# Performance work log

Hardware: AMD Instinct MI355X
Metric: run time of the kernel (lower is better)

The kernel has to match this reference:

```python
import jax, jax.numpy as jnp
import numpy as np
from jax.scipy.special import logsumexp

DEPTH = 7
LOG_EPS = jnp.float32(-64.0)
EPS = jnp.float32(np.exp(-64.0))


def leaf_interval(depth, start_idx=0):
    if depth == 0:
        return ([start_idx], [start_idx], [], start_idx)
    l_l, l_r, l_adj, last = leaf_interval(depth - 1, start_idx)
    my = last + 1
    r_l, r_r, r_adj, last = leaf_interval(depth - 1, my + 1)
    return ([my] + l_l, [my] + r_r,
            [(l, r) for l in l_r for r in r_l] + l_adj + r_adj, last)


_start, _end, _adj, _ = leaf_interval(DEPTH)
_out_idx = np.array([i for i, _ in _adj], dtype=np.int32)
OUT_UNIQ, OUT_INV = np.unique(_out_idx, return_inverse=True)
IN_IDX = np.array([j for _, j in _adj], dtype=np.int32)
START_IDXS = np.array(_start, dtype=np.int32)
END_IDXS = np.array(_end, dtype=np.int32)
N_STATES = 2 ** (DEPTH + 1) - 1  # 255


def log_safe(x):
    m = x < EPS
    return jnp.where(m, LOG_EPS, jnp.log(jnp.where(m, EPS, x)))


def exp_safe(x):
    m = x < LOG_EPS
    return jnp.where(m, EPS, jnp.exp(jnp.where(m, LOG_EPS, x)))


def setup_inputs() -> dict:
    key = jax.random.key(0)
    k1, k2, k3 = jax.random.split(key, 3)
    V, B, vocab, T = N_STATES, 64, 5000, 50
    log_probs = jax.nn.log_softmax(
        jax.random.normal(k1, (V, B, vocab), dtype=jnp.float32), axis=-1)
    targets = jax.random.randint(k2, (T, B), 0, vocab)
    target_lengths = jax.random.randint(k3, (B,), 1, T + 1)
    return {"log_probs": log_probs, "targets": targets,
            "target_lengths": target_lengths}


def _forward_ctreec(extracted, target_lengths):
    # extracted: [T, B, V] time-major per-state label log-probs
    T, B, V = extracted.shape
    out_uniq = jnp.asarray(OUT_UNIQ)
    out_inv = jnp.asarray(OUT_INV)
    in_idx = jnp.asarray(IN_IDX)
    end_idxs = jnp.asarray(END_IDXS)
    prev0 = jnp.zeros((B, V), jnp.float32).at[:, jnp.asarray(START_IDXS)].set(1.0)
    acc0 = jnp.zeros((B,), jnp.float32)

    def step(carry, xs):
        prev_probs, acc = carry
        elp_t, t = xs
        log_curr = log_safe(prev_probs) + elp_t            # [B, V]
        log_out = log_curr[:, out_uniq]                    # [B, U] unique out nodes
        log_C = logsumexp(log_out, axis=-1, keepdims=True)  # [B, 1]
        outgoing = exp_safe(log_out - log_C)[:, out_inv]   # [B, E] per-edge probs
        end = (t + 1) == target_lengths                    # [B]
        end_vals = logsumexp(log_curr[:, end_idxs], axis=1)
        acc = acc + jnp.where(end, end_vals, 0.0)
        mid = ((t + 1) < target_lengths) & (t < T - 1)
        acc = acc + jnp.where(mid, log_C[:, 0], 0.0)
        # scatter-add outgoing edge mass onto destination nodes
        new_prev = jnp.zeros_like(prev_probs).at[:, in_idx].add(outgoing)
        return (new_prev, acc), None

    (_, acc), _ = jax.lax.scan(step, (prev0, acc0),
                               (extracted, jnp.arange(T)))
    return acc


def reference(log_probs, targets, target_lengths):
    V, B, vocab = log_probs.shape
    # extracted[t, b, v] = log_probs[v, b, targets[t, b]]
    extracted = log_probs[:, jnp.arange(B)[None, :], targets]  # [V, T, B]
    extracted = jnp.transpose(extracted, (1, 2, 0))            # [T, B, V]
    return -_forward_ctreec(extracted, target_lengths)
```

## Files before the change

### kernel.cpp

```cpp
#include <hip/hip_runtime.h>
#include <math.h>


#define TT 50
#define BB 64
#define VOCAB 5000
#define NS 255
#define NSP 256
#define LOG_EPS_F (-64.0f)
#define EPS_F 1.6038109389511818e-28f
#define WS_NEEDED ((size_t)BB * TT * NSP * 4)

__device__ __forceinline__ float wred_sum(float x) {
#pragma unroll
    for (int m = 32; m >= 1; m >>= 1) x += __shfl_xor(x, m);
    return x;
}
__device__ __forceinline__ float wred_max(float x) {
#pragma unroll
    for (int m = 32; m >= 1; m >>= 1) x = fmaxf(x, __shfl_xor(x, m));
    return x;
}

__global__ __launch_bounds__(256) void gather_kernel(
    const float* __restrict__ log_probs,
    const int* __restrict__ targets,
    const int* __restrict__ target_lengths,
    float* __restrict__ ews)
{
    const int bt = blockIdx.x;
    const int b = bt / TT;
    const int t = bt % TT;
    if (t >= target_lengths[b]) return;
    const int v = threadIdx.x;
    const int tgt = targets[t * BB + b];
    float val = 0.0f;
    if (v < NS)
        val = __expf(log_probs[(size_t)v * (BB * VOCAB) + (size_t)b * VOCAB + tgt]);
    ews[(size_t)bt * NSP + v] = val;
}

__global__ __launch_bounds__(64) void scan_kernel(
    const float* __restrict__ ews,
    const int* __restrict__ target_lengths,
    float* __restrict__ out)
{
    const int b = blockIdx.x;
    const int lane = threadIdx.x;
    const int vbase = lane * 4;
    __shared__ float outv[NSP];

    const int len = target_lengths[b];
    const float4* ew = (const float4*)(ews + (size_t)b * TT * NSP);

    bool isend[4], isout[4];
    int kk[4], jj[4];
    float prev[4];
#pragma unroll
    for (int i = 0; i < 4; ++i) {
        int v = vbase + i;
        int p = v + 1;
        bool valid = (v < NS);
        bool pw2 = (p & (p - 1)) == 0;
        bool e_ = valid && ((p + (p & (-p))) == 256);
        isend[i] = e_;
        isout[i] = valid && !e_;
        prev[i] = (valid && pw2) ? 1.0f : 0.0f;
        if (valid && !pw2) {
            int s = __ffs(p) - 1;
            int q = p & (p - 1);
            kk[i] = __ffs(q) - 1;
            jj[i] = v - (1 << s);
        } else { kk[i] = 0; jj[i] = 0; }
    }

    float acc = 0.0f;
    float4 eA = ew[lane];
    float4 eB = (len > 1) ? ew[64 + lane] : eA;
    for (int t = 0; t < len; ++t) {
        float4 cur = eA;
        eA = eB;
        if (t + 2 < len) eB = ew[(t + 2) * 64 + lane];

        float c[4];
        c[0] = prev[0] * cur.x;
        c[1] = prev[1] * cur.y;
        c[2] = prev[2] * cur.z;
        c[3] = prev[3] * cur.w;

        if (t == len - 1) {
            float s = 0.0f;
#pragma unroll
            for (int i = 0; i < 4; ++i)
                if (isend[i]) s += c[i];
            s = wred_sum(s);
            acc += __logf(s);
        } else {
            *(float4*)&outv[vbase] = make_float4(c[0], c[1], c[2], c[3]);
            float s = 0.0f;
#pragma unroll
            for (int i = 0; i < 4; ++i)
                if (isout[i]) s += c[i];
            s = wred_sum(s);
            acc += __logf(s);
            float rinv = 1.0f / s;
            __syncthreads();
#pragma unroll
            for (int i = 0; i < 4; ++i) {
                float np_ = 0.0f;
                int bj = jj[i];
                int n = kk[i];
                for (int a = 0; a < n; ++a) np_ += outv[bj - (1 << a)];
                prev[i] = np_ * rinv;
            }
            __syncthreads();
        }
    }
    if (lane == 0) out[b] = -acc;
}

__global__ __launch_bounds__(64) void ctreec_fused(
    const float* __restrict__ log_probs,
    const int* __restrict__ targets,
    const int* __restrict__ target_lengths,
    float* __restrict__ out)
{
    const int b = blockIdx.x;
    const int lane = threadIdx.x;
    const int vbase = lane * 4;
    __shared__ float e_lds[TT * NSP];
    __shared__ float outv[NSP];
    __shared__ int tgts[TT];
    const int len = target_lengths[b];
    if (lane < TT) tgts[lane] = targets[lane * BB + b];
    __syncthreads();
    {
        const size_t bvoff = (size_t)b * VOCAB;
        float4* e_vec = (float4*)e_lds;
#pragma unroll 4
        for (int t = 0; t < len; ++t) {
            const float* base = log_probs + bvoff + (size_t)tgts[t];
            float4 val;
            val.x = base[(size_t)(vbase + 0) * (BB * VOCAB)];
            val.y = base[(size_t)(vbase + 1) * (BB * VOCAB)];
            val.z = base[(size_t)(vbase + 2) * (BB * VOCAB)];
            val.w = (vbase + 3 < NS) ? base[(size_t)(vbase + 3) * (BB * VOCAB)] : -1e30f;
            e_vec[t * 64 + lane] = val;
        }
    }
    __syncthreads();
    bool isend[4], isout[4];
    int kk[4], jj[4];
    float prev[4];
#pragma unroll
    for (int i = 0; i < 4; ++i) {
        int v = vbase + i;
        int p = v + 1;
        bool valid = (v < NS);
        bool pw2 = (p & (p - 1)) == 0;
        bool e_ = valid && ((p + (p & (-p))) == 256);
        isend[i] = e_;
        isout[i] = valid && !e_;
        prev[i] = (valid && pw2) ? 1.0f : 0.0f;
        if (valid && !pw2) {
            int s = __ffs(p) - 1;
            int q = p & (p - 1);
            kk[i] = __ffs(q) - 1;
            jj[i] = v - (1 << s);
        } else { kk[i] = 0; jj[i] = 0; }
    }
    const float4* e_vec = (const float4*)e_lds;
    float acc = 0.0f;
    for (int t = 0; t < len; ++t) {
        float4 e4 = e_vec[t * 64 + lane];
        float e[4] = {e4.x, e4.y, e4.z, e4.w};
        float lc[4];
#pragma unroll
        for (int i = 0; i < 4; ++i) {
            float pv = prev[i];
            float lp = (pv < EPS_F) ? LOG_EPS_F : __logf(pv);
            lc[i] = lp + e[i];
        }
        if (t == len - 1) {
            float m = -INFINITY;
#pragma unroll
            for (int i = 0; i < 4; ++i)
                if (isend[i]) m = fmaxf(m, lc[i]);
            m = wred_max(m);
            float s = 0.0f;
#pragma unroll
            for (int i = 0; i < 4; ++i)
                if (isend[i]) s += __expf(lc[i] - m);
            s = wred_sum(s);
            acc += m + __logf(s);
        } else {
            float m = -INFINITY;
#pragma unroll
            for (int i = 0; i < 4; ++i)
                if (isout[i]) m = fmaxf(m, lc[i]);
            m = wred_max(m);
            float s = 0.0f;
#pragma unroll
            for (int i = 0; i < 4; ++i)
                if (isout[i]) s += __expf(lc[i] - m);
            s = wred_sum(s);
            float logC = m + __logf(s);
            acc += logC;
#pragma unroll
            for (int i = 0; i < 4; ++i) {
                float d = lc[i] - logC;
                outv[vbase + i] = (d < LOG_EPS_F) ? EPS_F : __expf(d);
            }
            __syncthreads();
#pragma unroll
            for (int i = 0; i < 4; ++i) {
                float np_ = 0.0f;
                int bj = jj[i];
                int n = kk[i];
                for (int a = 0; a < n; ++a) np_ += outv[bj - (1 << a)];
                prev[i] = np_;
            }
            __syncthreads();
        }
    }
    if (lane == 0) out[b] = -acc;
}

extern "C" void kernel_launch(void* const* d_in, const int* in_sizes, int n_in,
                              void* d_out, int out_size, void* d_ws, size_t ws_size,
                              hipStream_t stream) {
    const float* log_probs = (const float*)d_in[0];
    const int* targets = (const int*)d_in[1];
    const int* target_lengths = (const int*)d_in[2];
    float* out = (float*)d_out;

    if (ws_size >= WS_NEEDED) {
        float* ews = (float*)d_ws;
        gather_kernel<<<dim3(BB * TT), dim3(256), 0, stream>>>(
            log_probs, targets, target_lengths, ews);
        scan_kernel<<<dim3(BB), dim3(64), 0, stream>>>(
            ews, target_lengths, out);
    } else {
        ctreec_fused<<<dim3(BB), dim3(64), 0, stream>>>(
            log_probs, targets, target_lengths, out);
    }
}
```

Before: 439.1 us.

## Fuse gather and linear-domain scan into one 512-thread kernel per batch

Replaces the two-kernel path (a gather into a global workspace followed by the scan) with a single kernel per batch element. Its 512 threads gather the exp'd per-state label probabilities straight into LDS, then one wave runs the linear-domain recurrence. Block-wide syncthreads in the recurrence become wave barriers, since only one wave remains. This removes the second launch and the global workspace round trip. The costs are only 64 blocks doing the scattered gather with a limited number of loads in flight, and about 51KB of LDS per block.

```diff
diff --git a/kernel.cpp b/kernel.cpp
--- a/kernel.cpp
+++ b/kernel.cpp
@@ -9,49 +9,50 @@
 #define NSP 256
 #define LOG_EPS_F (-64.0f)
 #define EPS_F 1.6038109389511818e-28f
-#define WS_NEEDED ((size_t)BB * TT * NSP * 4)
 
 __device__ __forceinline__ float wred_sum(float x) {
 #pragma unroll
     for (int m = 32; m >= 1; m >>= 1) x += __shfl_xor(x, m);
     return x;
 }
-__device__ __forceinline__ float wred_max(float x) {
-#pragma unroll
-    for (int m = 32; m >= 1; m >>= 1) x = fmaxf(x, __shfl_xor(x, m));
-    return x;
-}
 
-__global__ __launch_bounds__(256) void gather_kernel(
+__global__ __launch_bounds__(512) void ctreec_fused_lin(
     const float* __restrict__ log_probs,
     const int* __restrict__ targets,
-    const int* __restrict__ target_lengths,
-    float* __restrict__ ews)
-{
-    const int bt = blockIdx.x;
-    const int b = bt / TT;
-    const int t = bt % TT;
-    if (t >= target_lengths[b]) return;
-    const int v = threadIdx.x;
-    const int tgt = targets[t * BB + b];
-    float val = 0.0f;
-    if (v < NS)
-        val = __expf(log_probs[(size_t)v * (BB * VOCAB) + (size_t)b * VOCAB + tgt]);
-    ews[(size_t)bt * NSP + v] = val;
-}
-
-__global__ __launch_bounds__(64) void scan_kernel(
-    const float* __restrict__ ews,
     const int* __restrict__ target_lengths,
     float* __restrict__ out)
 {
     const int b = blockIdx.x;
-    const int lane = threadIdx.x;
-    const int vbase = lane * 4;
+    const int tid = threadIdx.x;
+
+    __shared__ float e_lds[TT * NSP];
     __shared__ float outv[NSP];
+    __shared__ int tgts[TT];
 
     const int len = target_lengths[b];
-    const float4* ew = (const float4*)(ews + (size_t)b * TT * NSP);
+
+    if (tid < TT) tgts[tid] = targets[tid * BB + b];
+    __syncthreads();
+
+    {
+        const int v = tid & (NSP - 1);
+        const int th = tid >> 8;
+        if (v < NS) {
+            const float* row =
+                log_probs + (size_t)v * (BB * VOCAB) + (size_t)b * VOCAB;
+            for (int t = th; t < len; t += 2)
+                e_lds[t * NSP + v] = __expf(row[tgts[t]]);
+        } else {
+            for (int t = th; t < len; t += 2)
+                e_lds[t * NSP + v] = 0.0f;
+        }
+    }
+    __syncthreads();
+
+    if (tid >= 64) return;
+
+    const int lane = tid;
+    const int vbase = lane * 4;
 
     bool isend[4], isout[4];
     int kk[4], jj[4];
@@ -74,13 +75,12 @@
         } else { kk[i] = 0; jj[i] = 0; }
     }
 
+    const float4* ev = (const float4*)e_lds;
     float acc = 0.0f;
-    float4 eA = ew[lane];
-    float4 eB = (len > 1) ? ew[64 + lane] : eA;
+    float4 eA = ev[lane];
     for (int t = 0; t < len; ++t) {
         float4 cur = eA;
-        eA = eB;
-        if (t + 2 < len) eB = ew[(t + 2) * 64 + lane];
+        if (t + 1 < len) eA = ev[(t + 1) * 64 + lane];
 
         float c[4];
         c[0] = prev[0] * cur.x;
@@ -104,7 +104,7 @@
             s = wred_sum(s);
             acc += __logf(s);
             float rinv = 1.0f / s;
-            __syncthreads();
+            __builtin_amdgcn_wave_barrier();
 #pragma unroll
             for (int i = 0; i < 4; ++i) {
                 float np_ = 0.0f;
@@ -113,114 +113,7 @@
                 for (int a = 0; a < n; ++a) np_ += outv[bj - (1 << a)];
                 prev[i] = np_ * rinv;
             }
-            __syncthreads();
-        }
-    }
-    if (lane == 0) out[b] = -acc;
-}
-
-__global__ __launch_bounds__(64) void ctreec_fused(
-    const float* __restrict__ log_probs,
-    const int* __restrict__ targets,
-    const int* __restrict__ target_lengths,
-    float* __restrict__ out)
-{
-    const int b = blockIdx.x;
-    const int lane = threadIdx.x;
-    const int vbase = lane * 4;
-    __shared__ float e_lds[TT * NSP];
-    __shared__ float outv[NSP];
-    __shared__ int tgts[TT];
-    const int len = target_lengths[b];
-    if (lane < TT) tgts[lane] = targets[lane * BB + b];
-    __syncthreads();
-    {
-        const size_t bvoff = (size_t)b * VOCAB;
-        float4* e_vec = (float4*)e_lds;
-#pragma unroll 4
-        for (int t = 0; t < len; ++t) {
-            const float* base = log_probs + bvoff + (size_t)tgts[t];
-            float4 val;
-            val.x = base[(size_t)(vbase + 0) * (BB * VOCAB)];
-            val.y = base[(size_t)(vbase + 1) * (BB * VOCAB)];
-            val.z = base[(size_t)(vbase + 2) * (BB * VOCAB)];
-            val.w = (vbase + 3 < NS) ? base[(size_t)(vbase + 3) * (BB * VOCAB)] : -1e30f;
-            e_vec[t * 64 + lane] = val;
-        }
-    }
-    __syncthreads();
-    bool isend[4], isout[4];
-    int kk[4], jj[4];
-    float prev[4];
-#pragma unroll
-    for (int i = 0; i < 4; ++i) {
-        int v = vbase + i;
-        int p = v + 1;
-        bool valid = (v < NS);
-        bool pw2 = (p & (p - 1)) == 0;
-        bool e_ = valid && ((p + (p & (-p))) == 256);
-        isend[i] = e_;
-        isout[i] = valid && !e_;
-        prev[i] = (valid && pw2) ? 1.0f : 0.0f;
-        if (valid && !pw2) {
-            int s = __ffs(p) - 1;
-            int q = p & (p - 1);
-            kk[i] = __ffs(q) - 1;
-            jj[i] = v - (1 << s);
-        } else { kk[i] = 0; jj[i] = 0; }
-    }
-    const float4* e_vec = (const float4*)e_lds;
-    float acc = 0.0f;
-    for (int t = 0; t < len; ++t) {
-        float4 e4 = e_vec[t * 64 + lane];
-        float e[4] = {e4.x, e4.y, e4.z, e4.w};
-        float lc[4];
-#pragma unroll
-        for (int i = 0; i < 4; ++i) {
-            float pv = prev[i];
-            float lp = (pv < EPS_F) ? LOG_EPS_F : __logf(pv);
-            lc[i] = lp + e[i];
-        }
-        if (t == len - 1) {
-            float m = -INFINITY;
-#pragma unroll
-            for (int i = 0; i < 4; ++i)
-                if (isend[i]) m = fmaxf(m, lc[i]);
-            m = wred_max(m);
-            float s = 0.0f;
-#pragma unroll
-            for (int i = 0; i < 4; ++i)
-                if (isend[i]) s += __expf(lc[i] - m);
-            s = wred_sum(s);
-            acc += m + __logf(s);
-        } else {
-            float m = -INFINITY;
-#pragma unroll
-            for (int i = 0; i < 4; ++i)
-                if (isout[i]) m = fmaxf(m, lc[i]);
-            m = wred_max(m);
-            float s = 0.0f;
-#pragma unroll
-            for (int i = 0; i < 4; ++i)
-                if (isout[i]) s += __expf(lc[i] - m);
-            s = wred_sum(s);
-            float logC = m + __logf(s);
-            acc += logC;
-#pragma unroll
-            for (int i = 0; i < 4; ++i) {
-                float d = lc[i] - logC;
-                outv[vbase + i] = (d < LOG_EPS_F) ? EPS_F : __expf(d);
-            }
-            __syncthreads();
-#pragma unroll
-            for (int i = 0; i < 4; ++i) {
-                float np_ = 0.0f;
-                int bj = jj[i];
-                int n = kk[i];
-                for (int a = 0; a < n; ++a) np_ += outv[bj - (1 << a)];
-                prev[i] = np_;
-            }
-            __syncthreads();
+            __builtin_amdgcn_wave_barrier();
         }
     }
     if (lane == 0) out[b] = -acc;
@@ -229,19 +122,12 @@
 extern "C" void kernel_launch(void* const* d_in, const int* in_sizes, int n_in,
                               void* d_out, int out_size, void* d_ws, size_t ws_size,
                               hipStream_t stream) {
+    (void)d_ws; (void)ws_size; (void)in_sizes; (void)n_in; (void)out_size;
     const float* log_probs = (const float*)d_in[0];
     const int* targets = (const int*)d_in[1];
     const int* target_lengths = (const int*)d_in[2];
     float* out = (float*)d_out;
 
-    if (ws_size >= WS_NEEDED) {
-        float* ews = (float*)d_ws;
-        gather_kernel<<<dim3(BB * TT), dim3(256), 0, stream>>>(
-            log_probs, targets, target_lengths, ews);
-        scan_kernel<<<dim3(BB), dim3(64), 0, stream>>>(
-            ews, target_lengths, out);
-    } else {
-        ctreec_fused<<<dim3(BB), dim3(64), 0, stream>>>(
-            log_probs, targets, target_lengths, out);
-    }
+    ctreec_fused_lin<<<dim3(BB), dim3(512), 0, stream>>>(
+        log_probs, targets, target_lengths, out);
 }
```

After: 454.9 us. +3.6%, slower.
